# Optimization experiments

Hardware: AMD Instinct MI355X
Metric: run time of the kernel (lower is better)

Reference implementation:

```python
import jax, jax.numpy as jnp
import numpy as np

FOUR_PI = 4.0 * np.pi
BIG = 1e10


def winding_numbers(points, tris):
    """Generalized winding number of `points` [B,N,3] w.r.t. triangle soup
    `tris` [B,F,3,3], via the Van Oosterom-Strackee solid-angle formula."""
    # vectors from each query point to the three triangle corners: [B,N,F,3]
    a = tris[:, None, :, 0, :] - points[:, :, None, :]
    b = tris[:, None, :, 1, :] - points[:, :, None, :]
    c = tris[:, None, :, 2, :] - points[:, :, None, :]
    la = jnp.linalg.norm(a, axis=-1)
    lb = jnp.linalg.norm(b, axis=-1)
    lc = jnp.linalg.norm(c, axis=-1)
    det = jnp.sum(a * jnp.cross(b, c), axis=-1)  # scalar triple product [B,N,F]
    denom = (la * lb * lc
             + jnp.sum(a * b, axis=-1) * lc
             + jnp.sum(b * c, axis=-1) * la
             + jnp.sum(c * a, axis=-1) * lb)
    omega = 2.0 * jnp.arctan2(det, denom)  # solid angle per triangle
    return jnp.sum(omega, axis=-1) / FOUR_PI  # [B,N]


def pairwise_dist(x, y):
    """Euclidean distances between clouds x [B,N1,3] and y [B,N2,3] -> [B,N1,N2]."""
    sq = (jnp.sum(x * x, -1)[:, :, None]
          + jnp.sum(y * y, -1)[:, None, :]
          - 2.0 * jnp.einsum('bnd,bmd->bnm', x, y))
    return jnp.sqrt(jnp.maximum(sq, 0.0))


def setup_inputs() -> dict:
    key = jax.random.key(0)
    k1, k2, k3 = jax.random.split(key, 3)
    B, N, F = 2, 6890, 3
    NF = 2000
    v1 = jax.random.normal(k1, (B, N, 3), dtype=jnp.float32)
    v2 = jax.random.normal(k2, (B, N, 3), dtype=jnp.float32) + 0.5
    faces = jax.random.randint(k3, (NF, 3), 0, N, dtype=jnp.int32)
    return {"v1": v1, "v2": v2, "faces": faces}


def _masked_stats(row_min, mask):
    # row_min [B,K] minimum distances; mask [B,K] interior flags
    any_in = jnp.any(mask, axis=1)                                   # [B]
    mx = jnp.max(jnp.where(mask, row_min, -BIG), axis=1)
    cnt = jnp.sum(mask, axis=1).astype(row_min.dtype)
    mn = jnp.sum(jnp.where(mask, row_min, 0.0), axis=1) / jnp.maximum(cnt, 1.0)
    zero = jnp.zeros_like(mx)
    return jnp.where(any_in, mx, zero), jnp.where(any_in, mn, zero)


def reference(v1, v2, faces):
    # triangle soups (no mouth-closing: 'smpl' path): [B,F,3,3]
    t1 = v1[:, faces, :]
    t2 = v2[:, faces, :]
    interior_v1 = winding_numbers(v1, t2) >= 0.99  # [B,N1]
    interior_v2 = winding_numbers(v2, t1) >= 0.99  # [B,N2]
    d = pairwise_dist(v1, v2)                      # [B,N1,N2]
    min_dist = jnp.min(d, axis=(1, 2))             # [B]
    row_min = jnp.min(d, axis=2)                   # [B,N1] dist of each v1 to v2
    col_min = jnp.min(d, axis=1)                   # [B,N2] dist of each v2 to v1
    max_12, mean_12 = _masked_stats(row_min, interior_v1)
    max_21, mean_21 = _masked_stats(col_min, interior_v2)
    # stacked [5,B]: min_dist, max_v1_in_v2, mean_v1_in_v2, max_v2_in_v1, mean_v2_in_v1
    return jnp.stack([min_dist, max_12, mean_12, max_21, mean_21], axis=0)
```

## Files before the change

kernel.cpp:

```cpp
#include <hip/hip_runtime.h>
#include <math.h>

#define B_     2
#define N_     6890
#define NF_    2000
#define NFP_   2048
#define NPT_   6912
#define OPP7_  7168
#define TCG_   16
#define OCG_   7
#define WTILE_ (4 * TCG_ * 27)
#define NTILE_ (4 * (TCG_ + OCG_) * 27)
#define GRID_  2048

typedef float v2f __attribute__((ext_vector_type(2)));
#define VFMA(a,b,c) __builtin_elementwise_fma((v2f)(a), (v2f)(b), (v2f)(c))

__device__ __forceinline__ float rotl1(float v) {
    return __int_as_float(__builtin_amdgcn_update_dpp(
        __float_as_int(v), __float_as_int(v), 0x134, 0xF, 0xF, false));
}

__device__ __forceinline__ float atan2_o2pi(float y, float x) {
    float ax = __builtin_fabsf(x);
    float ay = __builtin_fabsf(y);
    float mx = fmaxf(ax, ay);
    float mn = fminf(ax, ay);
    bool  big = mn > 0.41421356f * mx;
    float num = big ? (mn - mx) : mn;
    float den = big ? (mn + mx) : mx;
    float t   = num * __builtin_amdgcn_rcpf(den);
    float z   = t * t;
    float p   = fmaf(fmaf(fmaf(1.2817932e-2f, z, -2.2087019e-2f), z,
                          3.1795514e-2f), z, -5.3051037e-2f);
    float r   = fmaf(t, fmaf(z, p, 0.15915494309f), big ? 0.125f : 0.0f);
    r = (ay > ax)  ? 0.25f - r : r;
    r = (x < 0.0f) ? 0.5f  - r : r;
    return copysignf(r, y);
}

__global__ void prep_kernel(const float* __restrict__ v1, const float* __restrict__ v2,
                            const int* __restrict__ faces,
                            float4* __restrict__ pw1, float4* __restrict__ pw2,
                            float4* __restrict__ st1, float4* __restrict__ st2,
                            float* __restrict__ tbl1, float* __restrict__ tbl2,
                            int* __restrict__ cnt) {
    int tid = blockIdx.x * 256 + threadIdx.x;
    if (tid == 0) *cnt = 0;

    if (tid < B_ * NPT_) {
        int b = tid / NPT_, n = tid - b * NPT_;
        float4 q1 = make_float4(0.f, 0.f, 0.f, 0.f), q2 = q1;
        if (n < N_) {
            float x1 = v1[(b*N_+n)*3+0], y1 = v1[(b*N_+n)*3+1], z1 = v1[(b*N_+n)*3+2];
            float x2 = v2[(b*N_+n)*3+0], y2 = v2[(b*N_+n)*3+1], z2 = v2[(b*N_+n)*3+2];
            q1 = make_float4(x1, y1, z1, fmaf(x1,x1, fmaf(y1,y1, z1*z1)));
            q2 = make_float4(x2, y2, z2, fmaf(x2,x2, fmaf(y2,y2, z2*z2)));
        }
        pw1[tid] = q1; pw2[tid] = q2;
    }

    if (tid < B_ * OPP7_) {
        int b = tid / OPP7_, n = tid - b * OPP7_;
        float4 q1 = make_float4(0.f, 0.f, 0.f, 1e30f), q2 = q1;
        if (n < N_) {
            float x1 = v1[(b*N_+n)*3+0], y1 = v1[(b*N_+n)*3+1], z1 = v1[(b*N_+n)*3+2];
            float x2 = v2[(b*N_+n)*3+0], y2 = v2[(b*N_+n)*3+1], z2 = v2[(b*N_+n)*3+2];
            q1 = make_float4(-2.f*x1, -2.f*y1, -2.f*z1, fmaf(x1,x1, fmaf(y1,y1, z1*z1)));
            q2 = make_float4(-2.f*x2, -2.f*y2, -2.f*z2, fmaf(x2,x2, fmaf(y2,y2, z2*z2)));
        }
        st1[tid] = q1; st2[tid] = q2;
    }

    if (tid < 2 * B_ * NFP_) {
        int src = tid >> 12;
        int rr  = tid & (B_ * NFP_ - 1);
        int b   = rr >> 11;
        int f   = rr & (NFP_ - 1);
        const float* V = src ? v2 : v1;
        float Ax=1.f,Ay=1.f,Az=1.f,Bx=1.f,By=1.f,Bz=1.f,Cx=1.f,Cy=1.f,Cz=1.f;
        if (f < NF_) {
            int i0 = faces[f*3+0], i1 = faces[f*3+1], i2 = faces[f*3+2];
            Ax=V[(b*N_+i0)*3+0]; Ay=V[(b*N_+i0)*3+1]; Az=V[(b*N_+i0)*3+2];
            Bx=V[(b*N_+i1)*3+0]; By=V[(b*N_+i1)*3+1]; Bz=V[(b*N_+i1)*3+2];
            Cx=V[(b*N_+i2)*3+0]; Cy=V[(b*N_+i2)*3+1]; Cz=V[(b*N_+i2)*3+2];
        }
        float Sx = (Ay*Bz - Az*By) + (By*Cz - Bz*Cy) + (Cy*Az - Cz*Ay);
        float Sy = (Az*Bx - Ax*Bz) + (Bz*Cx - Bx*Cz) + (Cz*Ax - Cx*Az);
        float Sz = (Ax*By - Ay*Bx) + (Bx*Cy - By*Cx) + (Cx*Ay - Cy*Ax);
        float det0 = Ax*(By*Cz - Bz*Cy) + Ay*(Bz*Cx - Bx*Cz) + Az*(Bx*Cy - By*Cx);
        float na = Ax*Ax+Ay*Ay+Az*Az, nb = Bx*Bx+By*By+Bz*Bz, nc = Cx*Cx+Cy*Cy+Cz*Cz;
        float qab = Ax*Bx+Ay*By+Az*Bz, qbc = Bx*Cx+By*Cy+Bz*Cz, qca = Cx*Ax+Cy*Ay+Cz*Az;
        float* o = (src ? tbl2 : tbl1) + ((b << 11) + f) * 20;
        o[0]=Ax;  o[1]=Ay;  o[2]=Az;  o[3]=Bx;  o[4]=By;  o[5]=Bz;
        o[6]=Cx;  o[7]=Cy;  o[8]=Cz;  o[9]=-Sx; o[10]=-Sy; o[11]=-Sz;
        o[12]=det0; o[13]=na; o[14]=nb; o[15]=nc;
        o[16]=qab;  o[17]=qbc; o[18]=qca; o[19]=0.f;
    }
}

__global__ __launch_bounds__(256) void mega_kernel(
        const float4* __restrict__ pw1, const float4* __restrict__ pw2,
        const float* __restrict__ tbl1, const float* __restrict__ tbl2,
        const float4* __restrict__ st1, const float4* __restrict__ st2,
        float* __restrict__ part, float* __restrict__ rmp,
        int* __restrict__ cnt) {
    __shared__ float4 ptsd[512];
    __shared__ int stile;
    int t = threadIdx.x, wid = t >> 6, lane = t & 63;
    int pbase = (wid << 7) + lane;

    for (;;) {
        __syncthreads();
        if (t == 0) stile = atomicAdd(cnt, 1);
        __syncthreads();
        int tile = stile;
        if (tile >= NTILE_) break;

        if (tile < WTILE_) {
            int pgrp = tile % 27;
            int r    = tile / 27;
            int cg   = r & 15, db = r >> 4;
            int b = db & 1, dir = db >> 1;

            const float4* pw  = dir ? pw2 : pw1;
            const float*  tbl = dir ? tbl1 : tbl2;

            float4 P0 = pw[b * NPT_ + pgrp * 256 + t];
            ptsd[pbase]      = P0;
            ptsd[pbase + 64] = P0;

            const float4* rpA = (const float4*)(tbl + (size_t)(b*NFP_ + cg*128 +   0 + lane)*20);
            const float4* rpB = (const float4*)(tbl + (size_t)(b*NFP_ + cg*128 +  64 + lane)*20);
            float4 a0 = rpA[0], a1 = rpA[1], a2 = rpA[2], a3 = rpA[3], a4 = rpA[4];
            float4 b0 = rpB[0], b1 = rpB[1], b2 = rpB[2], b3 = rpB[3], b4 = rpB[4];
            v2f cAx = {a0.x,b0.x}, cAy = {a0.y,b0.y}, cAz = {a0.z,b0.z};
            v2f cBx = {a0.w,b0.w}, cBy = {a1.x,b1.x}, cBz = {a1.y,b1.y};
            v2f cCx = {a1.z,b1.z}, cCy = {a1.w,b1.w}, cCz = {a2.x,b2.x};
            v2f cSx = {a2.y,b2.y}, cSy = {a2.z,b2.z}, cSz = {a2.w,b2.w};
            v2f cD0 = {a3.x,b3.x}, cNa = {a3.y,b3.y}, cNb = {a3.z,b3.z}, cNc = {a3.w,b3.w};
            v2f cQab= {a4.x,b4.x}, cQbc= {a4.y,b4.y}, cQca= {a4.z,b4.z};

            const float4* mypts = ptsd + pbase;
            float acc = 0.f;
            #pragma unroll 4
            for (int k = 0; k < 64; ++k) {
                float4 P = mypts[k];
                v2f px = P.x, py = P.y, pz = P.z, sv = P.w;
                v2f dAp = VFMA(cAx, px, VFMA(cAy, py, cAz * pz));
                v2f dBp = VFMA(cBx, px, VFMA(cBy, py, cBz * pz));
                v2f dCp = VFMA(cCx, px, VFMA(cCy, py, cCz * pz));
                v2f det = VFMA(cSx, px, VFMA(cSy, py, VFMA(cSz, pz, cD0)));
                v2f la2 = VFMA((v2f)(-2.f), dAp, cNa + sv);
                v2f lb2 = VFMA((v2f)(-2.f), dBp, cNb + sv);
                v2f lc2 = VFMA((v2f)(-2.f), dCp, cNc + sv);
                v2f la, lb, lc;
                la.x = __builtin_amdgcn_sqrtf(fmaxf(la2.x, 0.f));
                la.y = __builtin_amdgcn_sqrtf(fmaxf(la2.y, 0.f));
                lb.x = __builtin_amdgcn_sqrtf(fmaxf(lb2.x, 0.f));
                lb.y = __builtin_amdgcn_sqrtf(fmaxf(lb2.y, 0.f));
                lc.x = __builtin_amdgcn_sqrtf(fmaxf(lc2.x, 0.f));
                lc.y = __builtin_amdgcn_sqrtf(fmaxf(lc2.y, 0.f));
                v2f dab = (cQab + sv) - (dAp + dBp);
                v2f dbc = (cQbc + sv) - (dBp + dCp);
                v2f dca = (cQca + sv) - (dCp + dAp);
                v2f denom = VFMA(VFMA(la, lb, dab), lc, VFMA(dbc, la, dca * lb));
                float g0 = atan2_o2pi(det.x, denom.x);
                float g1 = atan2_o2pi(det.y, denom.y);
                acc = rotl1(acc + (g0 + g1));
            }
            part[(db*TCG_ + cg)*NPT_ + pgrp*256 + t] = acc;
        } else {
            int rb   = tile - WTILE_;
            int pgrp = rb % 27;
            int r    = rb / 27;
            int ocg  = r % OCG_, db = r / OCG_;
            int b = db & 1, dir = db >> 1;

            const float4* pw = dir ? pw2 : pw1;
            const float4* st = dir ? st1 : st2;

            float4 P0 = pw[b * NPT_ + pgrp * 256 + t];
            ptsd[pbase]      = P0;
            ptsd[pbase + 64] = P0;

            const float4* qb = st + b * OPP7_ + ocg * 1024;
#define LQ(j) float4 q##j = qb[j*64 + lane];
            LQ(0) LQ(1) LQ(2) LQ(3) LQ(4) LQ(5) LQ(6) LQ(7)
            LQ(8) LQ(9) LQ(10) LQ(11) LQ(12) LQ(13) LQ(14) LQ(15)
#undef LQ

            const float4* mypts = ptsd + pbase;
            float m = 3.4e38f;
            #pragma unroll 2
            for (int k = 0; k < 64; ++k) {
                float4 P = mypts[k];
                float s = P.w;
#define DD(j) float d##j = fmaf(q##j.x,P.x, fmaf(q##j.y,P.y, fmaf(q##j.z,P.z, q##j.w)));
                DD(0) DD(1) DD(2) DD(3) DD(4) DD(5) DD(6) DD(7)
                DD(8) DD(9) DD(10) DD(11) DD(12) DD(13) DD(14) DD(15)
#undef DD
                float e0 = fminf(d0,d1),  e1 = fminf(d2,d3),  e2 = fminf(d4,d5),  e3 = fminf(d6,d7);
                float e4 = fminf(d8,d9),  e5 = fminf(d10,d11), e6 = fminf(d12,d13), e7 = fminf(d14,d15);
                float f0 = fminf(e0,e1), f1 = fminf(e2,e3), f2 = fminf(e4,e5), f3 = fminf(e6,e7);
                float h  = fminf(fminf(f0,f1), fminf(f2,f3));
                m = rotl1(fminf(m, h + s));
            }
            rmp[(db*OCG_ + ocg)*NPT_ + pgrp*256 + t] = m;
        }
    }
}

__global__ __launch_bounds__(256) void fold_kernel(
        const float* __restrict__ part, const float* __restrict__ rmp,
        float4* __restrict__ pstat) {
    int pg = blockIdx.x % 27, db = blockIdx.x / 27;
    int t = threadIdx.x, n = pg * 256 + t;

    float ws = 0.f;
    #pragma unroll
    for (int g = 0; g < TCG_; ++g) ws += part[(db*TCG_ + g)*NPT_ + n];
    float rv = 3.4e38f;
    #pragma unroll
    for (int g = 0; g < OCG_; ++g) rv = fminf(rv, rmp[(db*OCG_ + g)*NPT_ + n]);

    bool valid = n < N_;
    float d = sqrtf(rv);
    bool msk = valid && (ws >= 0.99f);
    float v_min = valid ? d : 3.4e38f;
    float v_max = msk ? d : -3.4e38f;
    float v_sum = msk ? d : 0.f;
    float v_cnt = msk ? 1.f : 0.f;

    #pragma unroll
    for (int off = 32; off; off >>= 1) {
        v_min = fminf(v_min, __shfl_down(v_min, off, 64));
        v_max = fmaxf(v_max, __shfl_down(v_max, off, 64));
        v_sum += __shfl_down(v_sum, off, 64);
        v_cnt += __shfl_down(v_cnt, off, 64);
    }
    __shared__ float4 sred[4];
    int wid = t >> 6, lane = t & 63;
    if (lane == 0) sred[wid] = make_float4(v_min, v_max, v_sum, v_cnt);
    __syncthreads();
    if (t == 0) {
        float4 a = sred[0], bb = sred[1], c = sred[2], dd = sred[3];
        pstat[db*27 + pg] = make_float4(
            fminf(fminf(a.x, bb.x), fminf(c.x, dd.x)),
            fmaxf(fmaxf(a.y, bb.y), fmaxf(c.y, dd.y)),
            (a.z + bb.z) + (c.z + dd.z),
            (a.w + bb.w) + (c.w + dd.w));
    }
}

__global__ void final_kernel(const float4* __restrict__ pstat, float* __restrict__ out) {
    int t = threadIdx.x, wid = t >> 6, lane = t & 63;
    float4 v = make_float4(3.4e38f, -3.4e38f, 0.f, 0.f);
    if (lane < 27) v = pstat[wid*27 + lane];
    #pragma unroll
    for (int off = 32; off; off >>= 1) {
        v.x = fminf(v.x, __shfl_down(v.x, off, 64));
        v.y = fmaxf(v.y, __shfl_down(v.y, off, 64));
        v.z += __shfl_down(v.z, off, 64);
        v.w += __shfl_down(v.w, off, 64);
    }
    __shared__ float4 res[4];
    if (lane == 0) res[wid] = v;
    __syncthreads();
    if (t == 0) {
        #pragma unroll
        for (int b = 0; b < B_; ++b) {
            float4 s1 = res[b], s2 = res[2 + b];
            out[0 + b] = s1.x;
            out[2 + b] = (s1.w > 0.f) ? s1.y : 0.f;
            out[4 + b] = (s1.w > 0.f) ? (s1.z / s1.w) : 0.f;
            out[6 + b] = (s2.w > 0.f) ? s2.y : 0.f;
            out[8 + b] = (s2.w > 0.f) ? (s2.z / s2.w) : 0.f;
        }
    }
}

extern "C" void kernel_launch(void* const* d_in, const int* in_sizes, int n_in,
                              void* d_out, int out_size, void* d_ws, size_t ws_size,
                              hipStream_t stream) {
    const float* v1    = (const float*)d_in[0];
    const float* v2    = (const float*)d_in[1];
    const int*   faces = (const int*)d_in[2];

    float4* f4 = (float4*)d_ws;
    float4* pw1   = f4;
    float4* pw2   = pw1 + B_ * NPT_;
    float4* st1   = pw2 + B_ * NPT_;
    float4* st2   = st1 + B_ * OPP7_;
    float4* pstat = st2 + B_ * OPP7_;
    float*  tbl1  = (float*)(pstat + 128);
    float*  tbl2  = tbl1 + B_ * NFP_ * 20;
    float*  part  = tbl2 + B_ * NFP_ * 20;
    float*  rmp   = part + 4 * TCG_ * NPT_;
    int*    cnt   = (int*)(rmp + 4 * OCG_ * NPT_);

    float* out = (float*)d_out;

    prep_kernel<<<(B_ * OPP7_ + 255) / 256, 256, 0, stream>>>(
        v1, v2, faces, pw1, pw2, st1, st2, tbl1, tbl2, cnt);

    mega_kernel<<<GRID_, 256, 0, stream>>>(
        pw1, pw2, tbl1, tbl2, st1, st2, part, rmp, cnt);

    fold_kernel<<<4 * 27, 256, 0, stream>>>(part, rmp, pstat);

    final_kernel<<<1, 256, 0, stream>>>(pstat, out);
}
```

Before: 113.7 us.

## Combine four solid angles per atan2 via complex products and drop atomic tile scheduler

Each thread now holds four triangles and merges their (det, denom) pairs by complex multiplication, so one atan2 per point replaces four. Integer branch-cut corrections restore the lost multiples of 2π. This sharply cuts transcendental and polynomial work in the winding-number loop, at the cost of extra multiplies, higher register pressure and possible overflow or precision loss in the products. The persistent atomic work queue is also replaced by a plain one-block-per-tile launch, which removes the counter reset and atomic traffic.

```diff
diff --git a/kernel.cpp b/kernel.cpp
--- a/kernel.cpp
+++ b/kernel.cpp
@@ -7,11 +7,10 @@
 #define NFP_   2048
 #define NPT_   6912
 #define OPP7_  7168
-#define TCG_   16
+#define TCG_   8
 #define OCG_   7
 #define WTILE_ (4 * TCG_ * 27)
 #define NTILE_ (4 * (TCG_ + OCG_) * 27)
-#define GRID_  2048
 
 typedef float v2f __attribute__((ext_vector_type(2)));
 #define VFMA(a,b,c) __builtin_elementwise_fma((v2f)(a), (v2f)(b), (v2f)(c))
@@ -39,14 +38,60 @@
     return copysignf(r, y);
 }
 
+__device__ __forceinline__ float corr(float y1, float y2, float yc) {
+    float c = (y1 > 0.f && y2 > 0.f && yc <= 0.f) ? 1.f : 0.f;
+    c = (y1 < 0.f && y2 < 0.f && yc >= 0.f) ? -1.f : c;
+    return c;
+}
+
+struct TriPack {
+    v2f Ax,Ay,Az,Bx,By,Bz,Cx,Cy,Cz,Sx,Sy,Sz,D0,Na,Nb,Nc,Qab,Qbc,Qca;
+};
+
+__device__ __forceinline__ TriPack packT(float4 a0, float4 a1, float4 a2,
+                                         float4 a3, float4 a4,
+                                         float4 b0, float4 b1, float4 b2,
+                                         float4 b3, float4 b4) {
+    TriPack T;
+    T.Ax = (v2f){a0.x,b0.x}; T.Ay = (v2f){a0.y,b0.y}; T.Az = (v2f){a0.z,b0.z};
+    T.Bx = (v2f){a0.w,b0.w}; T.By = (v2f){a1.x,b1.x}; T.Bz = (v2f){a1.y,b1.y};
+    T.Cx = (v2f){a1.z,b1.z}; T.Cy = (v2f){a1.w,b1.w}; T.Cz = (v2f){a2.x,b2.x};
+    T.Sx = (v2f){a2.y,b2.y}; T.Sy = (v2f){a2.z,b2.z}; T.Sz = (v2f){a2.w,b2.w};
+    T.D0 = (v2f){a3.x,b3.x}; T.Na = (v2f){a3.y,b3.y}; T.Nb = (v2f){a3.z,b3.z};
+    T.Nc = (v2f){a3.w,b3.w};
+    T.Qab= (v2f){a4.x,b4.x}; T.Qbc= (v2f){a4.y,b4.y}; T.Qca= (v2f){a4.z,b4.z};
+    return T;
+}
+
+__device__ __forceinline__ void chain(const TriPack& T, v2f px, v2f py, v2f pz,
+                                      v2f sv, v2f& yo, v2f& xo) {
+    v2f dAp = VFMA(T.Ax, px, VFMA(T.Ay, py, T.Az * pz));
+    v2f dBp = VFMA(T.Bx, px, VFMA(T.By, py, T.Bz * pz));
+    v2f dCp = VFMA(T.Cx, px, VFMA(T.Cy, py, T.Cz * pz));
+    v2f det = VFMA(T.Sx, px, VFMA(T.Sy, py, VFMA(T.Sz, pz, T.D0)));
+    v2f la2 = VFMA((v2f)(-2.f), dAp, T.Na + sv);
+    v2f lb2 = VFMA((v2f)(-2.f), dBp, T.Nb + sv);
+    v2f lc2 = VFMA((v2f)(-2.f), dCp, T.Nc + sv);
+    v2f la, lb, lc;
+    la.x = __builtin_amdgcn_sqrtf(fmaxf(la2.x, 0.f));
+    la.y = __builtin_amdgcn_sqrtf(fmaxf(la2.y, 0.f));
+    lb.x = __builtin_amdgcn_sqrtf(fmaxf(lb2.x, 0.f));
+    lb.y = __builtin_amdgcn_sqrtf(fmaxf(lb2.y, 0.f));
+    lc.x = __builtin_amdgcn_sqrtf(fmaxf(lc2.x, 0.f));
+    lc.y = __builtin_amdgcn_sqrtf(fmaxf(lc2.y, 0.f));
+    v2f dab = (T.Qab + sv) - (dAp + dBp);
+    v2f dbc = (T.Qbc + sv) - (dBp + dCp);
+    v2f dca = (T.Qca + sv) - (dCp + dAp);
+    xo = VFMA(VFMA(la, lb, dab), lc, VFMA(dbc, la, dca * lb));
+    yo = det;
+}
+
 __global__ void prep_kernel(const float* __restrict__ v1, const float* __restrict__ v2,
                             const int* __restrict__ faces,
                             float4* __restrict__ pw1, float4* __restrict__ pw2,
                             float4* __restrict__ st1, float4* __restrict__ st2,
-                            float* __restrict__ tbl1, float* __restrict__ tbl2,
-                            int* __restrict__ cnt) {
+                            float* __restrict__ tbl1, float* __restrict__ tbl2) {
     int tid = blockIdx.x * 256 + threadIdx.x;
-    if (tid == 0) *cnt = 0;
 
     if (tid < B_ * NPT_) {
         int b = tid / NPT_, n = tid - b * NPT_;
@@ -103,111 +148,89 @@
         const float4* __restrict__ pw1, const float4* __restrict__ pw2,
         const float* __restrict__ tbl1, const float* __restrict__ tbl2,
         const float4* __restrict__ st1, const float4* __restrict__ st2,
-        float* __restrict__ part, float* __restrict__ rmp,
-        int* __restrict__ cnt) {
+        float* __restrict__ part, float* __restrict__ rmp) {
     __shared__ float4 ptsd[512];
-    __shared__ int stile;
     int t = threadIdx.x, wid = t >> 6, lane = t & 63;
     int pbase = (wid << 7) + lane;
-
-    for (;;) {
-        __syncthreads();
-        if (t == 0) stile = atomicAdd(cnt, 1);
-        __syncthreads();
-        int tile = stile;
-        if (tile >= NTILE_) break;
-
-        if (tile < WTILE_) {
-            int pgrp = tile % 27;
-            int r    = tile / 27;
-            int cg   = r & 15, db = r >> 4;
-            int b = db & 1, dir = db >> 1;
-
-            const float4* pw  = dir ? pw2 : pw1;
-            const float*  tbl = dir ? tbl1 : tbl2;
-
-            float4 P0 = pw[b * NPT_ + pgrp * 256 + t];
-            ptsd[pbase]      = P0;
-            ptsd[pbase + 64] = P0;
-
-            const float4* rpA = (const float4*)(tbl + (size_t)(b*NFP_ + cg*128 +   0 + lane)*20);
-            const float4* rpB = (const float4*)(tbl + (size_t)(b*NFP_ + cg*128 +  64 + lane)*20);
-            float4 a0 = rpA[0], a1 = rpA[1], a2 = rpA[2], a3 = rpA[3], a4 = rpA[4];
-            float4 b0 = rpB[0], b1 = rpB[1], b2 = rpB[2], b3 = rpB[3], b4 = rpB[4];
-            v2f cAx = {a0.x,b0.x}, cAy = {a0.y,b0.y}, cAz = {a0.z,b0.z};
-            v2f cBx = {a0.w,b0.w}, cBy = {a1.x,b1.x}, cBz = {a1.y,b1.y};
-            v2f cCx = {a1.z,b1.z}, cCy = {a1.w,b1.w}, cCz = {a2.x,b2.x};
-            v2f cSx = {a2.y,b2.y}, cSy = {a2.z,b2.z}, cSz = {a2.w,b2.w};
-            v2f cD0 = {a3.x,b3.x}, cNa = {a3.y,b3.y}, cNb = {a3.z,b3.z}, cNc = {a3.w,b3.w};
-            v2f cQab= {a4.x,b4.x}, cQbc= {a4.y,b4.y}, cQca= {a4.z,b4.z};
-
-            const float4* mypts = ptsd + pbase;
-            float acc = 0.f;
-            #pragma unroll 4
-            for (int k = 0; k < 64; ++k) {
-                float4 P = mypts[k];
-                v2f px = P.x, py = P.y, pz = P.z, sv = P.w;
-                v2f dAp = VFMA(cAx, px, VFMA(cAy, py, cAz * pz));
-                v2f dBp = VFMA(cBx, px, VFMA(cBy, py, cBz * pz));
-                v2f dCp = VFMA(cCx, px, VFMA(cCy, py, cCz * pz));
-                v2f det = VFMA(cSx, px, VFMA(cSy, py, VFMA(cSz, pz, cD0)));
-                v2f la2 = VFMA((v2f)(-2.f), dAp, cNa + sv);
-                v2f lb2 = VFMA((v2f)(-2.f), dBp, cNb + sv);
-                v2f lc2 = VFMA((v2f)(-2.f), dCp, cNc + sv);
-                v2f la, lb, lc;
-                la.x = __builtin_amdgcn_sqrtf(fmaxf(la2.x, 0.f));
-                la.y = __builtin_amdgcn_sqrtf(fmaxf(la2.y, 0.f));
-                lb.x = __builtin_amdgcn_sqrtf(fmaxf(lb2.x, 0.f));
-                lb.y = __builtin_amdgcn_sqrtf(fmaxf(lb2.y, 0.f));
-                lc.x = __builtin_amdgcn_sqrtf(fmaxf(lc2.x, 0.f));
-                lc.y = __builtin_amdgcn_sqrtf(fmaxf(lc2.y, 0.f));
-                v2f dab = (cQab + sv) - (dAp + dBp);
-                v2f dbc = (cQbc + sv) - (dBp + dCp);
-                v2f dca = (cQca + sv) - (dCp + dAp);
-                v2f denom = VFMA(VFMA(la, lb, dab), lc, VFMA(dbc, la, dca * lb));
-                float g0 = atan2_o2pi(det.x, denom.x);
-                float g1 = atan2_o2pi(det.y, denom.y);
-                acc = rotl1(acc + (g0 + g1));
-            }
-            part[(db*TCG_ + cg)*NPT_ + pgrp*256 + t] = acc;
-        } else {
-            int rb   = tile - WTILE_;
-            int pgrp = rb % 27;
-            int r    = rb / 27;
-            int ocg  = r % OCG_, db = r / OCG_;
-            int b = db & 1, dir = db >> 1;
-
-            const float4* pw = dir ? pw2 : pw1;
-            const float4* st = dir ? st1 : st2;
-
-            float4 P0 = pw[b * NPT_ + pgrp * 256 + t];
-            ptsd[pbase]      = P0;
-            ptsd[pbase + 64] = P0;
-
-            const float4* qb = st + b * OPP7_ + ocg * 1024;
+    int tile = blockIdx.x;
+
+    if (tile < WTILE_) {
+        int pgrp = tile % 27;
+        int r    = tile / 27;
+        int cg   = r & 7, db = r >> 3;
+        int b = db & 1, dir = db >> 1;
+
+        const float4* pw  = dir ? pw2 : pw1;
+        const float*  tbl = dir ? tbl1 : tbl2;
+
+        float4 P0 = pw[b * NPT_ + pgrp * 256 + t];
+        ptsd[pbase]      = P0;
+        ptsd[pbase + 64] = P0;
+
+        const float4* rp0 = (const float4*)(tbl + (size_t)(b*NFP_ + cg*256 +   0 + lane)*20);
+        const float4* rp1 = (const float4*)(tbl + (size_t)(b*NFP_ + cg*256 +  64 + lane)*20);
+        const float4* rp2 = (const float4*)(tbl + (size_t)(b*NFP_ + cg*256 + 128 + lane)*20);
+        const float4* rp3 = (const float4*)(tbl + (size_t)(b*NFP_ + cg*256 + 192 + lane)*20);
+        TriPack TA = packT(rp0[0],rp0[1],rp0[2],rp0[3],rp0[4],
+                           rp1[0],rp1[1],rp1[2],rp1[3],rp1[4]);
+        TriPack TB = packT(rp2[0],rp2[1],rp2[2],rp2[3],rp2[4],
+                           rp3[0],rp3[1],rp3[2],rp3[3],rp3[4]);
+
+        const float4* mypts = ptsd + pbase;
+        float acc = 0.f;
+        #pragma unroll 2
+        for (int k = 0; k < 64; ++k) {
+            float4 P = mypts[k];
+            v2f px = P.x, py = P.y, pz = P.z, sv = P.w;
+            v2f yA, xA, yB, xB;
+            chain(TA, px, py, pz, sv, yA, xA);
+            chain(TB, px, py, pz, sv, yB, xB);
+            v2f yP = VFMA(yA, xB, yB * xA);
+            v2f xP = VFMA(-yA, yB, xA * xB);
+            float c01 = corr(yA.x, yB.x, yP.x) + corr(yA.y, yB.y, yP.y);
+            float yT = fmaf(yP.x, xP.y, yP.y * xP.x);
+            float xT = fmaf(-yP.x, yP.y, xP.x * xP.y);
+            float c2 = corr(yP.x, yP.y, yT);
+            acc = rotl1(acc + (atan2_o2pi(yT, xT) + (c01 + c2)));
+        }
+        part[(db*TCG_ + cg)*NPT_ + pgrp*256 + t] = acc;
+    } else {
+        int rb   = tile - WTILE_;
+        int pgrp = rb % 27;
+        int r    = rb / 27;
+        int ocg  = r % OCG_, db = r / OCG_;
+        int b = db & 1, dir = db >> 1;
+
+        const float4* pw = dir ? pw2 : pw1;
+        const float4* st = dir ? st1 : st2;
+
+        float4 P0 = pw[b * NPT_ + pgrp * 256 + t];
+        ptsd[pbase]      = P0;
+        ptsd[pbase + 64] = P0;
+
+        const float4* qb = st + b * OPP7_ + ocg * 1024;
 #define LQ(j) float4 q##j = qb[j*64 + lane];
-            LQ(0) LQ(1) LQ(2) LQ(3) LQ(4) LQ(5) LQ(6) LQ(7)
-            LQ(8) LQ(9) LQ(10) LQ(11) LQ(12) LQ(13) LQ(14) LQ(15)
+        LQ(0) LQ(1) LQ(2) LQ(3) LQ(4) LQ(5) LQ(6) LQ(7)
+        LQ(8) LQ(9) LQ(10) LQ(11) LQ(12) LQ(13) LQ(14) LQ(15)
 #undef LQ
 
-            const float4* mypts = ptsd + pbase;
-            float m = 3.4e38f;
-            #pragma unroll 2
-            for (int k = 0; k < 64; ++k) {
-                float4 P = mypts[k];
-                float s = P.w;
+        const float4* mypts = ptsd + pbase;
+        float m = 3.4e38f;
+        #pragma unroll 2
+        for (int k = 0; k < 64; ++k) {
+            float4 P = mypts[k];
+            float s = P.w;
 #define DD(j) float d##j = fmaf(q##j.x,P.x, fmaf(q##j.y,P.y, fmaf(q##j.z,P.z, q##j.w)));
-                DD(0) DD(1) DD(2) DD(3) DD(4) DD(5) DD(6) DD(7)
-                DD(8) DD(9) DD(10) DD(11) DD(12) DD(13) DD(14) DD(15)
+            DD(0) DD(1) DD(2) DD(3) DD(4) DD(5) DD(6) DD(7)
+            DD(8) DD(9) DD(10) DD(11) DD(12) DD(13) DD(14) DD(15)
 #undef DD
-                float e0 = fminf(d0,d1),  e1 = fminf(d2,d3),  e2 = fminf(d4,d5),  e3 = fminf(d6,d7);
-                float e4 = fminf(d8,d9),  e5 = fminf(d10,d11), e6 = fminf(d12,d13), e7 = fminf(d14,d15);
-                float f0 = fminf(e0,e1), f1 = fminf(e2,e3), f2 = fminf(e4,e5), f3 = fminf(e6,e7);
-                float h  = fminf(fminf(f0,f1), fminf(f2,f3));
-                m = rotl1(fminf(m, h + s));
-            }
-            rmp[(db*OCG_ + ocg)*NPT_ + pgrp*256 + t] = m;
-        }
+            float e0 = fminf(d0,d1),  e1 = fminf(d2,d3),  e2 = fminf(d4,d5),  e3 = fminf(d6,d7);
+            float e4 = fminf(d8,d9),  e5 = fminf(d10,d11), e6 = fminf(d12,d13), e7 = fminf(d14,d15);
+            float f0 = fminf(e0,e1), f1 = fminf(e2,e3), f2 = fminf(e4,e5), f3 = fminf(e6,e7);
+            float h  = fminf(fminf(f0,f1), fminf(f2,f3));
+            m = rotl1(fminf(m, h + s));
+        }
+        rmp[(db*OCG_ + ocg)*NPT_ + pgrp*256 + t] = m;
     }
 }
 
@@ -297,15 +320,14 @@
     float*  tbl2  = tbl1 + B_ * NFP_ * 20;
     float*  part  = tbl2 + B_ * NFP_ * 20;
     float*  rmp   = part + 4 * TCG_ * NPT_;
-    int*    cnt   = (int*)(rmp + 4 * OCG_ * NPT_);
 
     float* out = (float*)d_out;
 
     prep_kernel<<<(B_ * OPP7_ + 255) / 256, 256, 0, stream>>>(
-        v1, v2, faces, pw1, pw2, st1, st2, tbl1, tbl2, cnt);
-
-    mega_kernel<<<GRID_, 256, 0, stream>>>(
-        pw1, pw2, tbl1, tbl2, st1, st2, part, rmp, cnt);
+        v1, v2, faces, pw1, pw2, st1, st2, tbl1, tbl2);
+
+    mega_kernel<<<NTILE_, 256, 0, stream>>>(
+        pw1, pw2, tbl1, tbl2, st1, st2, part, rmp);
 
     fold_kernel<<<4 * 27, 256, 0, stream>>>(part, rmp, pstat);
 
```

Result: faster. 91.39 us (-19.6%).
